# Performance work log

Measured on AMD Instinct MI355X. Metric: run time of the kernel, lower is better.

## Reference

```python
import jax, jax.numpy as jnp
import numpy as np

B, S, E, H = 16, 256, 4096, 16
D = E // H  # 256; module's matmul pattern requires S == D and B == H


def setup_inputs() -> dict:
    rng = jax.random.key(0)
    k0, k1, k2, k3, k4 = jax.random.split(rng, 5)
    return {
        "query": jax.random.normal(k0, (B, S, E), jnp.float32),
        "key": jax.random.normal(k1, (B, S, E), jnp.float32),
        "value": jax.random.normal(k2, (B, S, E), jnp.float32),
        # out_proj: torch nn.Linear(E, E) -> y = x @ W.T + b
        "out_w": jax.random.normal(k3, (E, E), jnp.float32) * 0.02,
        "out_b": jnp.zeros((E,), jnp.float32),
    }


def reference(query, key, value, out_w, out_b):
    scale = D ** -0.5
    # split heads: [B, S, E] -> [B, H, S, D]
    q = (query * scale).reshape(B, S, H, D).transpose(0, 2, 1, 3)
    k = key.reshape(B, S, H, D).transpose(0, 2, 1, 3)
    v = value.reshape(B, S, H, D).transpose(0, 2, 1, 3)
    # torch.matmul(q_head, k_head) with NO transpose: contracts q's D with k's S
    # (valid because S == D). aw: [B, H, S, D]
    aw = jnp.einsum('bhit,bhtj->bhij', q, k)
    # attn_weights.transpose(0, 1): [B, H, ...] -> [H, B, ...]
    aw = jnp.swapaxes(aw, 0, 1)
    # eval mode path: softmax over last dim (no dropout)
    aw = jax.nn.softmax(aw, axis=-1)
    # torch.matmul(aw [H,B,S,D], v [B,H,S,D]): batch dims broadcast because B == H,
    # pairing elementwise -> out[x,y] = aw[x,y] @ v[x,y]
    out = jnp.einsum('xyit,xytj->xyij', aw, v)
    # transpose(1, 2) then reshape to (B, S, E)
    out = jnp.swapaxes(out, 1, 2).reshape(B, S, E)
    # out_proj
    return out @ out_w.T + out_b
```

## Files before the change

kernel.cpp:

```cpp
#include <hip/hip_runtime.h>

#define AS1 __attribute__((address_space(1)))
#define AS3 __attribute__((address_space(3)))

typedef __bf16 bf16x8 __attribute__((ext_vector_type(8)));
typedef float f32x4 __attribute__((ext_vector_type(4)));

__device__ __forceinline__ unsigned short f2bf(float f) {
  unsigned int u = __builtin_bit_cast(unsigned int, f);
  u += 0x7fffu + ((u >> 16) & 1u);
  return (unsigned short)(u >> 16);
}

__global__ __launch_bounds__(256) void kv_transpose(
    const float* __restrict__ key, const float* __restrict__ value,
    unsigned short* __restrict__ KT2, unsigned short* __restrict__ VT2) {
  __shared__ float tr[32 * 33];
  const int tid = threadIdx.x;
  const int ts  = blockIdx.y;
  const int pp  = blockIdx.x >> 3;
  const int s   = blockIdx.x & 7;
  const int b   = ts ? (pp >> 4) : (pp & 15);
  const int h   = ts ? (pp & 15) : (pp >> 4);
  const float* src = (ts ? value : key) + ((size_t)(b * 256 + s * 32)) * 4096 + h * 256;
  unsigned short* dst = (ts ? VT2 : KT2) + (size_t)(pp * 8 + s) * 8192;
  const int tt = tid >> 3;
  const int q8 = tid & 7;
  for (int jb = 0; jb < 8; ++jb) {
    float4 v = *(const float4*)(src + (size_t)tt * 4096 + jb * 32 + q8 * 4);
    tr[tt * 33 + q8 * 4 + 0] = v.x;
    tr[tt * 33 + q8 * 4 + 1] = v.y;
    tr[tt * 33 + q8 * 4 + 2] = v.z;
    tr[tt * 33 + q8 * 4 + 3] = v.w;
    __syncthreads();
    ushort4 o;
    o.x = f2bf(tr[(q8 * 4 + 0) * 33 + tt]);
    o.y = f2bf(tr[(q8 * 4 + 1) * 33 + tt]);
    o.z = f2bf(tr[(q8 * 4 + 2) * 33 + tt]);
    o.w = f2bf(tr[(q8 * 4 + 3) * 33 + tt]);
    *(ushort4*)(dst + (jb * 32 + tt) * 32 + q8 * 4) = o;
    __syncthreads();
  }
}

__global__ __launch_bounds__(256, 2) void attn_convw(
    const float* __restrict__ qin, const unsigned short* __restrict__ KT2,
    const unsigned short* __restrict__ VT2, unsigned short* __restrict__ attn,
    const float* __restrict__ w, unsigned short* __restrict__ wbf,
    int nattn) {
  const int tid = threadIdx.x;
  int bid = blockIdx.x;

  if (bid >= nattn) {
    const int b2 = bid - nattn;
#pragma unroll
    for (int it = 0; it < 8; ++it) {
      const int flat = b2 * 16384 + it * 2048 + tid * 8;
      const float4* s = (const float4*)(w + flat);
      float4 v0 = s[0], v1 = s[1];
      uint4 pk;
      pk.x = (unsigned)f2bf(v0.x) | ((unsigned)f2bf(v0.y) << 16);
      pk.y = (unsigned)f2bf(v0.z) | ((unsigned)f2bf(v0.w) << 16);
      pk.z = (unsigned)f2bf(v1.x) | ((unsigned)f2bf(v1.y) << 16);
      pk.w = (unsigned)f2bf(v1.z) | ((unsigned)f2bf(v1.w) << 16);
      *(uint4*)(wbf + flat) = pk;
    }
    return;
  }

  __shared__ __align__(16) unsigned short kv[8192];
  __shared__ __align__(16) unsigned short plds[4 * 16 * 264];

  const int lane = tid & 63;
  const int wave = tid >> 6;
  const int li   = lane & 15;
  const int ks   = lane >> 4;

  const int pp  = (bid & 7) * 32 + ((bid >> 3) & 31);
  const int ib  = bid >> 8;
  const int x = pp >> 4, y = pp & 15;
  const int i0 = ib * 64 + wave * 16;

  bf16x8 qf[8];
  {
    const float* qrow = qin + ((size_t)(y * 256 + i0 + li)) * 4096 + x * 256 + ks * 8;
#pragma unroll
    for (int s = 0; s < 8; ++s) {
      float4 v0 = *(const float4*)(qrow + s * 32);
      float4 v1 = *(const float4*)(qrow + s * 32 + 4);
      union { bf16x8 v; unsigned short u[8]; } t;
      t.u[0] = f2bf(v0.x * 0.0625f); t.u[1] = f2bf(v0.y * 0.0625f);
      t.u[2] = f2bf(v0.z * 0.0625f); t.u[3] = f2bf(v0.w * 0.0625f);
      t.u[4] = f2bf(v1.x * 0.0625f); t.u[5] = f2bf(v1.y * 0.0625f);
      t.u[6] = f2bf(v1.z * 0.0625f); t.u[7] = f2bf(v1.w * 0.0625f);
      qf[s] = t.v;
    }
  }

  const f32x4 vzero = {0.f, 0.f, 0.f, 0.f};
  f32x4 sacc[16];
#pragma unroll
  for (int f = 0; f < 16; ++f) sacc[f] = vzero;

  const unsigned short* ktile = KT2 + (size_t)pp * 65536;
#pragma unroll
  for (int s = 0; s < 8; ++s) {
    __syncthreads();
#pragma unroll
    for (int cc = 0; cc < 4; ++cc) {
      const unsigned short* g = ktile + (size_t)s * 8192 + (cc * 256 + tid) * 8;
      __builtin_amdgcn_global_load_lds((AS1 unsigned int*)g,
          (AS3 unsigned int*)((AS3 char*)kv + cc * 4096 + wave * 1024), 16, 0, 0);
    }
    __syncthreads();
#pragma unroll
    for (int f = 0; f < 16; ++f) {
      bf16x8 bfr = *(const bf16x8*)&kv[(f * 16 + li) * 32 + ks * 8];
      sacc[f] = __builtin_amdgcn_mfma_f32_16x16x32_bf16(qf[s], bfr, sacc[f], 0, 0, 0);
    }
  }

  float sm[4];
#pragma unroll
  for (int qi = 0; qi < 4; ++qi) {
    float m = sacc[0][qi];
#pragma unroll
    for (int f = 1; f < 16; ++f) m = fmaxf(m, sacc[f][qi]);
    m = fmaxf(m, __shfl_xor(m, 1));
    m = fmaxf(m, __shfl_xor(m, 2));
    m = fmaxf(m, __shfl_xor(m, 4));
    m = fmaxf(m, __shfl_xor(m, 8));
    float ssum = 0.f;
#pragma unroll
    for (int f = 0; f < 16; ++f) {
      float pv = __expf(sacc[f][qi] - m);
      sacc[f][qi] = pv;
      ssum += pv;
    }
    ssum += __shfl_xor(ssum, 1);
    ssum += __shfl_xor(ssum, 2);
    ssum += __shfl_xor(ssum, 4);
    ssum += __shfl_xor(ssum, 8);
    sm[qi] = ssum;
  }

  unsigned short* pw = plds + wave * 4224;
#pragma unroll
  for (int f = 0; f < 16; ++f)
#pragma unroll
    for (int qi = 0; qi < 4; ++qi)
      pw[(ks * 4 + qi) * 264 + f * 16 + li] = f2bf(sacc[f][qi]);

  f32x4 oacc[16];
#pragma unroll
  for (int f = 0; f < 16; ++f) oacc[f] = vzero;
  const unsigned short* vtile = VT2 + (size_t)pp * 65536;
  const unsigned short* pr = plds + wave * 4224 + li * 264;
#pragma unroll
  for (int s2 = 0; s2 < 8; ++s2) {
    __syncthreads();
#pragma unroll
    for (int cc = 0; cc < 4; ++cc) {
      const unsigned short* g = vtile + (size_t)s2 * 8192 + (cc * 256 + tid) * 8;
      __builtin_amdgcn_global_load_lds((AS1 unsigned int*)g,
          (AS3 unsigned int*)((AS3 char*)kv + cc * 4096 + wave * 1024), 16, 0, 0);
    }
    __syncthreads();
    bf16x8 afr = *(const bf16x8*)&pr[s2 * 32 + ks * 8];
#pragma unroll
    for (int f = 0; f < 16; ++f) {
      bf16x8 bfr = *(const bf16x8*)&kv[(f * 16 + li) * 32 + ks * 8];
      oacc[f] = __builtin_amdgcn_mfma_f32_16x16x32_bf16(afr, bfr, oacc[f], 0, 0, 0);
    }
  }

  float rs4[4];
#pragma unroll
  for (int qi = 0; qi < 4; ++qi) rs4[qi] = 1.0f / sm[qi];
  unsigned short* abase = attn + (size_t)(x * 256 + i0 + ks * 4) * 4096 + y * 256 + li;
#pragma unroll
  for (int f = 0; f < 16; ++f)
#pragma unroll
    for (int qi = 0; qi < 4; ++qi)
      abase[(size_t)qi * 4096 + f * 16] = f2bf(oacc[f][qi] * rs4[qi]);
}

__global__ __launch_bounds__(256) void convw(const float* __restrict__ w,
                                             unsigned short* __restrict__ o) {
  const int i = blockIdx.x * 256 + threadIdx.x;
  const float4* s = (const float4*)w + (size_t)i * 2;
  float4 v0 = s[0], v1 = s[1];
  uint4 pk;
  pk.x = (unsigned)f2bf(v0.x) | ((unsigned)f2bf(v0.y) << 16);
  pk.y = (unsigned)f2bf(v0.z) | ((unsigned)f2bf(v0.w) << 16);
  pk.z = (unsigned)f2bf(v1.x) | ((unsigned)f2bf(v1.y) << 16);
  pk.w = (unsigned)f2bf(v1.z) | ((unsigned)f2bf(v1.w) << 16);
  *((uint4*)o + i) = pk;
}

__global__ __launch_bounds__(512, 2) void proj_gemm64(
    const unsigned short* __restrict__ A, const unsigned short* __restrict__ W,
    const float* __restrict__ bias, float* __restrict__ out) {
  __shared__ __align__(1024) char lds[131072];

  const int tid  = threadIdx.x;
  const int lane = tid & 63;
  const int w    = tid >> 6;
  const int li   = lane & 15;
  const int ks   = lane >> 4;
  const int wr   = w >> 2;
  const int wc   = w & 3;
  const int LB   = (li * 64 + ks * 16) ^ (((li >> 3) & 1) << 5);

  const int bid = blockIdx.x;
  const int swz = (bid & 7) * 32 + (bid >> 3);
  const int m0b = (swz >> 4) * 256, n0b = (swz & 15) * 256;

  unsigned sA[2], sB[2];
  int dstP[2];
#pragma unroll
  for (int j = 0; j < 2; ++j) {
    int P = j * 8192 + tid * 16;
    int L = P ^ (((P >> 9) & 1) << 5);
    int row = L >> 6, col = L & 63;
    dstP[j] = P;
    sA[j] = (unsigned)((m0b + row) * 8192 + col);
    sB[j] = (unsigned)((n0b + row) * 8192 + col);
  }
  const char* Ac = (const char*)A;
  const char* Wc = (const char*)W;
  AS3 char* L3 = (AS3 char*)lds;

  const f32x4 vzero = {0.f, 0.f, 0.f, 0.f};
  f32x4 acc[8][4];
#pragma unroll
  for (int m = 0; m < 8; ++m)
#pragma unroll
    for (int n = 0; n < 4; ++n) acc[m][n] = vzero;

#define STG_A(kt, buf, kk) do {                                                \
    const unsigned _o = (unsigned)(kt) * 128u + (unsigned)(kk) * 64u;          \
    _Pragma("unroll") for (int j = 0; j < 2; ++j)                              \
      __builtin_amdgcn_global_load_lds((AS1 unsigned int*)(Ac + sA[j] + _o),   \
          (AS3 unsigned int*)(L3 + (buf) + (kk) * 16384 + dstP[j]), 16, 0, 0); \
  } while (0)
#define STG_B(kt, buf, kk) do {                                                \
    const unsigned _o = (unsigned)(kt) * 128u + (unsigned)(kk) * 64u;          \
    _Pragma("unroll") for (int j = 0; j < 2; ++j)                              \
      __builtin_amdgcn_global_load_lds((AS1 unsigned int*)(Wc + sB[j] + _o),   \
          (AS3 unsigned int*)(L3 + (buf) + 32768 + (kk) * 16384 + dstP[j]),    \
          16, 0, 0);                                                           \
  } while (0)
#define RD_A(buf, kk, m) (*(const bf16x8*)(lds + (buf) + (kk) * 16384 +        \
                                           wr * 8192 + (m) * 1024 + LB))
#define RD_B(buf, kk, n) (*(const bf16x8*)(lds + (buf) + 32768 + (kk) * 16384 + \
                                           wc * 4096 + (n) * 1024 + LB))
#define MFMA(a, b, c) __builtin_amdgcn_mfma_f32_16x16x32_bf16((a), (b), (c), 0, 0, 0)

  STG_A(0, 0, 0); STG_A(0, 0, 1); STG_B(0, 0, 0); STG_B(0, 0, 1);
  asm volatile("s_waitcnt vmcnt(0)" ::: "memory");
  __builtin_amdgcn_s_barrier();

  for (int t = 0; t < 64; ++t) {
    const int cur = (t & 1) * 65536;
    const int oth = 65536 - cur;
    const int k1  = (t < 63) ? t + 1 : 63;
    bf16x8 af[8], bf[4];

    STG_A(k1, oth, 0); STG_A(k1, oth, 1);
    af[0] = RD_A(cur, 0, 0);
#pragma unroll
    for (int n = 0; n < 4; ++n) bf[n] = RD_B(cur, 0, n);
#pragma unroll
    for (int m = 1; m < 8; ++m) af[m] = RD_A(cur, 0, m);
    __builtin_amdgcn_s_setprio(1);
#pragma unroll
    for (int m = 0; m < 8; ++m)
#pragma unroll
      for (int n = 0; n < 4; ++n)
        acc[m][n] = MFMA(af[m], bf[n], acc[m][n]);
    __builtin_amdgcn_s_setprio(0);

    STG_B(k1, oth, 0); STG_B(k1, oth, 1);
    af[0] = RD_A(cur, 1, 0);
#pragma unroll
    for (int n = 0; n < 4; ++n) bf[n] = RD_B(cur, 1, n);
#pragma unroll
    for (int m = 1; m < 8; ++m) af[m] = RD_A(cur, 1, m);
    __builtin_amdgcn_s_setprio(1);
#pragma unroll
    for (int m = 0; m < 8; ++m)
#pragma unroll
      for (int n = 0; n < 4; ++n)
        acc[m][n] = MFMA(af[m], bf[n], acc[m][n]);
    __builtin_amdgcn_s_setprio(0);

    asm volatile("s_waitcnt vmcnt(0)" ::: "memory");
    __builtin_amdgcn_s_barrier();
  }

  float bv[4];
#pragma unroll
  for (int n = 0; n < 4; ++n) bv[n] = bias[n0b + wc * 64 + n * 16 + li];
#pragma unroll
  for (int m = 0; m < 8; ++m) {
#pragma unroll
    for (int qi = 0; qi < 4; ++qi) {
      const int row = m0b + wr * 128 + m * 16 + ks * 4 + qi;
      float* orow = out + (size_t)row * 4096 + n0b + wc * 64 + li;
#pragma unroll
      for (int n = 0; n < 4; ++n) orow[n * 16] = acc[m][n][qi] + bv[n];
    }
  }
#undef STG_A
#undef STG_B
#undef RD_A
#undef RD_B
#undef MFMA
}

extern "C" void kernel_launch(void* const* d_in, const int* in_sizes, int n_in,
                              void* d_out, int out_size, void* d_ws, size_t ws_size,
                              hipStream_t stream) {
  const float* q = (const float*)d_in[0];
  const float* k = (const float*)d_in[1];
  const float* v = (const float*)d_in[2];
  const float* w = (const float*)d_in[3];
  const float* b = (const float*)d_in[4];
  float* out = (float*)d_out;
  char* ws = (char*)d_ws;

  unsigned short* attn = (unsigned short*)ws;
  unsigned short* KT2  = (unsigned short*)(ws + (size_t)33554432);
  unsigned short* VT2  = (unsigned short*)(ws + (size_t)67108864);

  kv_transpose<<<dim3(2048, 2), 256, 0, stream>>>(k, v, KT2, VT2);

  if (ws_size >= (size_t)134217728) {
    unsigned short* wbf = (unsigned short*)(ws + (size_t)100663296);
    attn_convw<<<2048, 256, 0, stream>>>(q, KT2, VT2, attn, w, wbf, 1024);
    proj_gemm64<<<256, 512, 0, stream>>>(attn, wbf, b, out);
  } else {
    unsigned short* wbf = KT2;
    attn_convw<<<1024, 256, 0, stream>>>(q, KT2, VT2, attn, w, wbf, 1024);
    convw<<<8192, 256, 0, stream>>>(w, wbf);
    proj_gemm64<<<256, 512, 0, stream>>>(attn, wbf, b, out);
  }
}
```

Baseline: 221.6 us.

## Switch projection GEMM to 32x32x16 MFMA tiles with new LDS swizzle

```diff
diff --git a/kernel.cpp b/kernel.cpp
--- a/kernel.cpp
+++ b/kernel.cpp
@@ -5,6 +5,7 @@
 
 typedef __bf16 bf16x8 __attribute__((ext_vector_type(8)));
 typedef float f32x4 __attribute__((ext_vector_type(4)));
+typedef float f32x16 __attribute__((ext_vector_type(16)));
 
 __device__ __forceinline__ unsigned short f2bf(float f) {
   unsigned int u = __builtin_bit_cast(unsigned int, f);
@@ -198,7 +199,7 @@
   *((uint4*)o + i) = pk;
 }
 
-__global__ __launch_bounds__(512, 2) void proj_gemm64(
+__global__ __launch_bounds__(512, 2) void proj_gemm32(
     const unsigned short* __restrict__ A, const unsigned short* __restrict__ W,
     const float* __restrict__ bias, float* __restrict__ out) {
   __shared__ __align__(1024) char lds[131072];
@@ -206,11 +207,11 @@
   const int tid  = threadIdx.x;
   const int lane = tid & 63;
   const int w    = tid >> 6;
-  const int li   = lane & 15;
-  const int ks   = lane >> 4;
+  const int l31  = lane & 31;
+  const int lhi  = lane >> 5;
   const int wr   = w >> 2;
   const int wc   = w & 3;
-  const int LB   = (li * 64 + ks * 16) ^ (((li >> 3) & 1) << 5);
+  const int colLane = ((lhi) << 4) ^ ((lane & 3) << 4);
 
   const int bid = blockIdx.x;
   const int swz = (bid & 7) * 32 + (bid >> 3);
@@ -221,22 +222,23 @@
 #pragma unroll
   for (int j = 0; j < 2; ++j) {
     int P = j * 8192 + tid * 16;
-    int L = P ^ (((P >> 9) & 1) << 5);
-    int row = L >> 6, col = L & 63;
+    int row = P >> 6;
+    int cb  = (P & 63) ^ ((row & 3) << 4);
     dstP[j] = P;
-    sA[j] = (unsigned)((m0b + row) * 8192 + col);
-    sB[j] = (unsigned)((n0b + row) * 8192 + col);
+    sA[j] = (unsigned)((m0b + row) * 8192 + cb);
+    sB[j] = (unsigned)((n0b + row) * 8192 + cb);
   }
   const char* Ac = (const char*)A;
   const char* Wc = (const char*)W;
   AS3 char* L3 = (AS3 char*)lds;
 
-  const f32x4 vzero = {0.f, 0.f, 0.f, 0.f};
-  f32x4 acc[8][4];
-#pragma unroll
-  for (int m = 0; m < 8; ++m)
-#pragma unroll
-    for (int n = 0; n < 4; ++n) acc[m][n] = vzero;
+  f32x16 acc[4][2];
+#pragma unroll
+  for (int mi = 0; mi < 4; ++mi)
+#pragma unroll
+    for (int ni = 0; ni < 2; ++ni)
+#pragma unroll
+      for (int r = 0; r < 16; ++r) acc[mi][ni][r] = 0.f;
 
 #define STG_A(kt, buf, kk) do {                                                \
     const unsigned _o = (unsigned)(kt) * 128u + (unsigned)(kk) * 64u;          \
@@ -251,11 +253,11 @@
           (AS3 unsigned int*)(L3 + (buf) + 32768 + (kk) * 16384 + dstP[j]),    \
           16, 0, 0);                                                           \
   } while (0)
-#define RD_A(buf, kk, m) (*(const bf16x8*)(lds + (buf) + (kk) * 16384 +        \
-                                           wr * 8192 + (m) * 1024 + LB))
-#define RD_B(buf, kk, n) (*(const bf16x8*)(lds + (buf) + 32768 + (kk) * 16384 + \
-                                           wc * 4096 + (n) * 1024 + LB))
-#define MFMA(a, b, c) __builtin_amdgcn_mfma_f32_16x16x32_bf16((a), (b), (c), 0, 0, 0)
+#define RD_A(buf, kk, c, mi) (*(const bf16x8*)(lds + (buf) + (kk) * 16384 +    \
+    (wr * 128 + (mi) * 32 + l31) * 64 + (((c) << 5) ^ colLane)))
+#define RD_B(buf, kk, c, ni) (*(const bf16x8*)(lds + (buf) + 32768 +           \
+    (kk) * 16384 + (wc * 64 + (ni) * 32 + l31) * 64 + (((c) << 5) ^ colLane)))
+#define MFMA32(a, b, c) __builtin_amdgcn_mfma_f32_32x32x16_bf16((a), (b), (c), 0, 0, 0)
 
   STG_A(0, 0, 0); STG_A(0, 0, 1); STG_B(0, 0, 0); STG_B(0, 0, 1);
   asm volatile("s_waitcnt vmcnt(0)" ::: "memory");
@@ -265,58 +267,63 @@
     const int cur = (t & 1) * 65536;
     const int oth = 65536 - cur;
     const int k1  = (t < 63) ? t + 1 : 63;
-    bf16x8 af[8], bf[4];
-
-    STG_A(k1, oth, 0); STG_A(k1, oth, 1);
-    af[0] = RD_A(cur, 0, 0);
-#pragma unroll
-    for (int n = 0; n < 4; ++n) bf[n] = RD_B(cur, 0, n);
-#pragma unroll
-    for (int m = 1; m < 8; ++m) af[m] = RD_A(cur, 0, m);
-    __builtin_amdgcn_s_setprio(1);
-#pragma unroll
-    for (int m = 0; m < 8; ++m)
-#pragma unroll
-      for (int n = 0; n < 4; ++n)
-        acc[m][n] = MFMA(af[m], bf[n], acc[m][n]);
-    __builtin_amdgcn_s_setprio(0);
-
-    STG_B(k1, oth, 0); STG_B(k1, oth, 1);
-    af[0] = RD_A(cur, 1, 0);
-#pragma unroll
-    for (int n = 0; n < 4; ++n) bf[n] = RD_B(cur, 1, n);
-#pragma unroll
-    for (int m = 1; m < 8; ++m) af[m] = RD_A(cur, 1, m);
-    __builtin_amdgcn_s_setprio(1);
-#pragma unroll
-    for (int m = 0; m < 8; ++m)
-#pragma unroll
-      for (int n = 0; n < 4; ++n)
-        acc[m][n] = MFMA(af[m], bf[n], acc[m][n]);
-    __builtin_amdgcn_s_setprio(0);
+    bf16x8 af0[4], bf0[2], af1[4], bf1[2];
+
+#pragma unroll
+    for (int kk = 0; kk < 2; ++kk) {
+      if (kk == 0) { STG_A(k1, oth, 0); STG_A(k1, oth, 1); }
+      else         { STG_B(k1, oth, 0); STG_B(k1, oth, 1); }
+
+      af0[0] = RD_A(cur, kk, 0, 0);
+      bf0[0] = RD_B(cur, kk, 0, 0);
+      bf0[1] = RD_B(cur, kk, 0, 1);
+#pragma unroll
+      for (int mi = 1; mi < 4; ++mi) af0[mi] = RD_A(cur, kk, 0, mi);
+      af1[0] = RD_A(cur, kk, 1, 0);
+      bf1[0] = RD_B(cur, kk, 1, 0);
+      bf1[1] = RD_B(cur, kk, 1, 1);
+#pragma unroll
+      for (int mi = 1; mi < 4; ++mi) af1[mi] = RD_A(cur, kk, 1, mi);
+
+      __builtin_amdgcn_s_setprio(1);
+#pragma unroll
+      for (int mi = 0; mi < 4; ++mi)
+#pragma unroll
+        for (int ni = 0; ni < 2; ++ni)
+          acc[mi][ni] = MFMA32(af0[mi], bf0[ni], acc[mi][ni]);
+#pragma unroll
+      for (int mi = 0; mi < 4; ++mi)
+#pragma unroll
+        for (int ni = 0; ni < 2; ++ni)
+          acc[mi][ni] = MFMA32(af1[mi], bf1[ni], acc[mi][ni]);
+      __builtin_amdgcn_s_setprio(0);
+    }
 
     asm volatile("s_waitcnt vmcnt(0)" ::: "memory");
     __builtin_amdgcn_s_barrier();
   }
 
-  float bv[4];
-#pragma unroll
-  for (int n = 0; n < 4; ++n) bv[n] = bias[n0b + wc * 64 + n * 16 + li];
-#pragma unroll
-  for (int m = 0; m < 8; ++m) {
-#pragma unroll
-    for (int qi = 0; qi < 4; ++qi) {
-      const int row = m0b + wr * 128 + m * 16 + ks * 4 + qi;
-      float* orow = out + (size_t)row * 4096 + n0b + wc * 64 + li;
-#pragma unroll
-      for (int n = 0; n < 4; ++n) orow[n * 16] = acc[m][n][qi] + bv[n];
+  float bv2[2];
+#pragma unroll
+  for (int ni = 0; ni < 2; ++ni) bv2[ni] = bias[n0b + wc * 64 + ni * 32 + l31];
+#pragma unroll
+  for (int mi = 0; mi < 4; ++mi) {
+#pragma unroll
+    for (int ni = 0; ni < 2; ++ni) {
+      const int rb = m0b + wr * 128 + mi * 32 + 4 * lhi;
+      float* ob = out + (size_t)rb * 4096 + n0b + wc * 64 + ni * 32 + l31;
+#pragma unroll
+      for (int r = 0; r < 16; ++r) {
+        const int rowoff = (r & 3) + 8 * (r >> 2);
+        ob[(size_t)rowoff * 4096] = acc[mi][ni][r] + bv2[ni];
+      }
     }
   }
 #undef STG_A
 #undef STG_B
 #undef RD_A
 #undef RD_B
-#undef MFMA
+#undef MFMA32
 }
 
 extern "C" void kernel_launch(void* const* d_in, const int* in_sizes, int n_in,
@@ -339,11 +346,11 @@
   if (ws_size >= (size_t)134217728) {
     unsigned short* wbf = (unsigned short*)(ws + (size_t)100663296);
     attn_convw<<<2048, 256, 0, stream>>>(q, KT2, VT2, attn, w, wbf, 1024);
-    proj_gemm64<<<256, 512, 0, stream>>>(attn, wbf, b, out);
+    proj_gemm32<<<256, 512, 0, stream>>>(attn, wbf, b, out);
   } else {
     unsigned short* wbf = KT2;
     attn_convw<<<1024, 256, 0, stream>>>(q, KT2, VT2, attn, w, wbf, 1024);
     convw<<<8192, 256, 0, stream>>>(w, wbf);
-    proj_gemm64<<<256, 512, 0, stream>>>(attn, wbf, b, out);
-  }
-}
+    proj_gemm32<<<256, 512, 0, stream>>>(attn, wbf, b, out);
+  }
+}
```

After: 253.4 us. +14.4%, slower.

## Store attention output in MFMA-fragment order and load A directly to registers

Applied to the files above, without the earlier changes.

```diff
diff --git a/kernel.cpp b/kernel.cpp
--- a/kernel.cpp
+++ b/kernel.cpp
@@ -10,6 +10,10 @@
   unsigned int u = __builtin_bit_cast(unsigned int, f);
   u += 0x7fffu + ((u >> 16) & 1u);
   return (unsigned short)(u >> 16);
+}
+
+__device__ __forceinline__ bf16x8 asbf(uint4 v) {
+  bf16x8 r; __builtin_memcpy(&r, &v, 16); return r;
 }
 
 __global__ __launch_bounds__(256) void kv_transpose(
@@ -177,12 +181,17 @@
   float rs4[4];
 #pragma unroll
   for (int qi = 0; qi < 4; ++qi) rs4[qi] = 1.0f / sm[qi];
-  unsigned short* abase = attn + (size_t)(x * 256 + i0 + ks * 4) * 4096 + y * 256 + li;
-#pragma unroll
-  for (int f = 0; f < 16; ++f)
+  const int rb  = x * 16 + ib * 4 + wave;
+  const int li3 = li >> 3;
+  const int le  = li & 7;
+#pragma unroll
+  for (int f = 0; f < 16; ++f) {
+    const size_t cbase = ((size_t)rb * 128 + y * 8 + (f >> 1)) * 512
+                       + (size_t)((((f << 1) + li3) & 3) * 16) * 8 + le;
 #pragma unroll
     for (int qi = 0; qi < 4; ++qi)
-      abase[(size_t)qi * 4096 + f * 16] = f2bf(oacc[f][qi] * rs4[qi]);
+      attn[cbase + (ks * 4 + qi) * 8] = f2bf(oacc[f][qi] * rs4[qi]);
+  }
 }
 
 __global__ __launch_bounds__(256) void convw(const float* __restrict__ w,
@@ -198,10 +207,10 @@
   *((uint4*)o + i) = pk;
 }
 
-__global__ __launch_bounds__(512, 2) void proj_gemm64(
+__global__ __launch_bounds__(512, 2) void proj_gemm_af(
     const unsigned short* __restrict__ A, const unsigned short* __restrict__ W,
     const float* __restrict__ bias, float* __restrict__ out) {
-  __shared__ __align__(1024) char lds[131072];
+  __shared__ __align__(1024) char lds[65536];
 
   const int tid  = threadIdx.x;
   const int lane = tid & 63;
@@ -216,7 +225,7 @@
   const int swz = (bid & 7) * 32 + (bid >> 3);
   const int m0b = (swz >> 4) * 256, n0b = (swz & 15) * 256;
 
-  unsigned sA[2], sB[2];
+  unsigned sB[2];
   int dstP[2];
 #pragma unroll
   for (int j = 0; j < 2; ++j) {
@@ -224,13 +233,14 @@
     int L = P ^ (((P >> 9) & 1) << 5);
     int row = L >> 6, col = L & 63;
     dstP[j] = P;
-    sA[j] = (unsigned)((m0b + row) * 8192 + col);
     sB[j] = (unsigned)((n0b + row) * 8192 + col);
   }
-  const char* Ac = (const char*)A;
   const char* Wc = (const char*)W;
   AS3 char* L3 = (AS3 char*)lds;
 
+  const char* Ap = (const char*)A;
+  const size_t aB = (size_t)((swz >> 4) * 16 + wr * 8) * 131072 + (size_t)lane * 16;
+
   const f32x4 vzero = {0.f, 0.f, 0.f, 0.f};
   f32x4 acc[8][4];
 #pragma unroll
@@ -238,64 +248,58 @@
 #pragma unroll
     for (int n = 0; n < 4; ++n) acc[m][n] = vzero;
 
-#define STG_A(kt, buf, kk) do {                                                \
-    const unsigned _o = (unsigned)(kt) * 128u + (unsigned)(kk) * 64u;          \
-    _Pragma("unroll") for (int j = 0; j < 2; ++j)                              \
-      __builtin_amdgcn_global_load_lds((AS1 unsigned int*)(Ac + sA[j] + _o),   \
-          (AS3 unsigned int*)(L3 + (buf) + (kk) * 16384 + dstP[j]), 16, 0, 0); \
-  } while (0)
 #define STG_B(kt, buf, kk) do {                                                \
     const unsigned _o = (unsigned)(kt) * 128u + (unsigned)(kk) * 64u;          \
     _Pragma("unroll") for (int j = 0; j < 2; ++j)                              \
       __builtin_amdgcn_global_load_lds((AS1 unsigned int*)(Wc + sB[j] + _o),   \
-          (AS3 unsigned int*)(L3 + (buf) + 32768 + (kk) * 16384 + dstP[j]),    \
-          16, 0, 0);                                                           \
+          (AS3 unsigned int*)(L3 + (buf) + (kk) * 16384 + dstP[j]), 16, 0, 0); \
   } while (0)
-#define RD_A(buf, kk, m) (*(const bf16x8*)(lds + (buf) + (kk) * 16384 +        \
-                                           wr * 8192 + (m) * 1024 + LB))
-#define RD_B(buf, kk, n) (*(const bf16x8*)(lds + (buf) + 32768 + (kk) * 16384 + \
+#define RD_B(buf, kk, n) (*(const bf16x8*)(lds + (buf) + (kk) * 16384 +        \
                                            wc * 4096 + (n) * 1024 + LB))
+#define LDA(DST, kc) do {                                                      \
+    _Pragma("unroll") for (int mi = 0; mi < 8; ++mi)                           \
+      DST[mi] = *(const uint4*)(Ap + aB + (size_t)mi * 131072 +                \
+                                (size_t)(kc) * 1024);                          \
+  } while (0)
 #define MFMA(a, b, c) __builtin_amdgcn_mfma_f32_16x16x32_bf16((a), (b), (c), 0, 0, 0)
 
-  STG_A(0, 0, 0); STG_A(0, 0, 1); STG_B(0, 0, 0); STG_B(0, 0, 1);
+  uint4 Aa[8], Ab[8];
+
+  STG_B(0, 0, 0); STG_B(0, 0, 1);
+  LDA(Aa, 0);
   asm volatile("s_waitcnt vmcnt(0)" ::: "memory");
   __builtin_amdgcn_s_barrier();
 
   for (int t = 0; t < 64; ++t) {
-    const int cur = (t & 1) * 65536;
-    const int oth = 65536 - cur;
+    const int cur = (t & 1) * 32768;
+    const int oth = 32768 - cur;
     const int k1  = (t < 63) ? t + 1 : 63;
-    bf16x8 af[8], bf[4];
-
-    STG_A(k1, oth, 0); STG_A(k1, oth, 1);
-    af[0] = RD_A(cur, 0, 0);
+    bf16x8 bf[4];
+
+    LDA(Ab, 2 * t + 1);
 #pragma unroll
     for (int n = 0; n < 4; ++n) bf[n] = RD_B(cur, 0, n);
-#pragma unroll
-    for (int m = 1; m < 8; ++m) af[m] = RD_A(cur, 0, m);
     __builtin_amdgcn_s_setprio(1);
 #pragma unroll
     for (int m = 0; m < 8; ++m)
 #pragma unroll
       for (int n = 0; n < 4; ++n)
-        acc[m][n] = MFMA(af[m], bf[n], acc[m][n]);
+        acc[m][n] = MFMA(asbf(Aa[m]), bf[n], acc[m][n]);
     __builtin_amdgcn_s_setprio(0);
 
     STG_B(k1, oth, 0); STG_B(k1, oth, 1);
-    af[0] = RD_A(cur, 1, 0);
+    LDA(Aa, 2 * k1);
 #pragma unroll
     for (int n = 0; n < 4; ++n) bf[n] = RD_B(cur, 1, n);
-#pragma unroll
-    for (int m = 1; m < 8; ++m) af[m] = RD_A(cur, 1, m);
     __builtin_amdgcn_s_setprio(1);
 #pragma unroll
     for (int m = 0; m < 8; ++m)
 #pragma unroll
       for (int n = 0; n < 4; ++n)
-        acc[m][n] = MFMA(af[m], bf[n], acc[m][n]);
+        acc[m][n] = MFMA(asbf(Ab[m]), bf[n], acc[m][n]);
     __builtin_amdgcn_s_setprio(0);
 
-    asm volatile("s_waitcnt vmcnt(0)" ::: "memory");
+    asm volatile("s_waitcnt vmcnt(8)" ::: "memory");
     __builtin_amdgcn_s_barrier();
   }
 
@@ -312,10 +316,9 @@
       for (int n = 0; n < 4; ++n) orow[n * 16] = acc[m][n][qi] + bv[n];
     }
   }
-#undef STG_A
 #undef STG_B
-#undef RD_A
 #undef RD_B
+#undef LDA
 #undef MFMA
 }
 
@@ -339,11 +342,11 @@
   if (ws_size >= (size_t)134217728) {
     unsigned short* wbf = (unsigned short*)(ws + (size_t)100663296);
     attn_convw<<<2048, 256, 0, stream>>>(q, KT2, VT2, attn, w, wbf, 1024);
-    proj_gemm64<<<256, 512, 0, stream>>>(attn, wbf, b, out);
+    proj_gemm_af<<<256, 512, 0, stream>>>(attn, wbf, b, out);
   } else {
     unsigned short* wbf = KT2;
     attn_convw<<<1024, 256, 0, stream>>>(q, KT2, VT2, attn, w, wbf, 1024);
     convw<<<8192, 256, 0, stream>>>(w, wbf);
-    proj_gemm64<<<256, 512, 0, stream>>>(attn, wbf, b, out);
-  }
-}
+    proj_gemm_af<<<256, 512, 0, stream>>>(attn, wbf, b, out);
+  }
+}
```

New measurement: 234.8 us. 1.06x slower.
